# Kernel optimization log

Hardware: AMD Instinct MI355X
Metric: run time of the kernel (lower is better)

## Reference

```python
import jax, jax.numpy as jnp
import numpy as np

B, T, C, H = 2, 2048, 1024, 16
D = C // H  # head dim = 64


def setup_inputs() -> dict:
    key = jax.random.key(0)
    ks = jax.random.split(key, 9)
    s = 1.0 / np.sqrt(C)
    x = jax.random.normal(ks[0], (B, T, C), dtype=jnp.float32)
    # causal lower-triangular mask, broadcast over heads: [B, 1, T, T]
    attn_mask = jnp.broadcast_to(jnp.tril(jnp.ones((T, T), dtype=jnp.int32)), (B, 1, T, T))
    Wq = jax.random.normal(ks[1], (C, C), dtype=jnp.float32) * s
    Wk = jax.random.normal(ks[2], (C, C), dtype=jnp.float32) * s
    Wv = jax.random.normal(ks[3], (C, C), dtype=jnp.float32) * s
    Wo = jax.random.normal(ks[4], (C, C), dtype=jnp.float32) * s
    bq = jax.random.normal(ks[5], (C,), dtype=jnp.float32) * s
    bk = jax.random.normal(ks[6], (C,), dtype=jnp.float32) * s
    bv = jax.random.normal(ks[7], (C,), dtype=jnp.float32) * s
    bo = jax.random.normal(ks[8], (C,), dtype=jnp.float32) * s
    return {"x": x, "attn_mask": attn_mask, "Wq": Wq, "bq": bq, "Wk": Wk, "bk": bk,
            "Wv": Wv, "bv": bv, "Wo": Wo, "bo": bo}


def reference(x, attn_mask, Wq, bq, Wk, bk, Wv, bv, Wo, bo):
    # Q/K/V projections: nn.Linear applies x @ W^T + b
    def split_heads(t):  # [B,T,C] -> [B,H,T,D]
        return t.reshape(B, T, H, D).transpose(0, 2, 1, 3)

    q = split_heads(x @ Wq.T + bq)
    k = split_heads(x @ Wk.T + bk)
    v = split_heads(x @ Wv.T + bv)

    scale = 1.0 / np.sqrt(D)
    att = jnp.einsum('bhqd,bhkd->bhqk', q, k) * scale  # [B,H,T,T]
    att = jnp.where(attn_mask[:, :, :T, :T] == 0, -jnp.inf, att)
    att = jax.nn.softmax(att, axis=-1)
    # dropout p=0.0 -> identity
    y = jnp.einsum('bhqk,bhkd->bhqd', att, v)  # [B,H,T,D]
    y = y.transpose(0, 2, 1, 3).reshape(B, T, C)
    return y @ Wo.T + bo
```

## Files before the change

kernel.cpp:

```cpp
#include <hip/hip_runtime.h>
#include <hip/hip_bf16.h>

#define B_ 2
#define T_ 2048
#define C_ 1024
#define H_ 16
#define D_ 64
#define BT_ (B_ * T_)
#define S3_ 3072

typedef __bf16 bf16x8 __attribute__((ext_vector_type(8)));
typedef short short8v __attribute__((ext_vector_type(8)));
typedef short s16x4 __attribute__((ext_vector_type(4)));
typedef float f32x4 __attribute__((ext_vector_type(4)));

__device__ inline bf16x8 ld_frag_bf(const short* p) {
    short8v s = *(const short8v*)p;
    return __builtin_bit_cast(bf16x8, s);
}
__device__ inline short f2bf(float f) {
    union { float f; unsigned u; } x;
    x.f = f;
    unsigned r = x.u + 0x7fff + ((x.u >> 16) & 1);
    return (short)(r >> 16);
}
__device__ inline void st_out(short* p, float v) { *p = f2bf(v); }
__device__ inline void st_out(float* p, float v) { *p = v; }

__device__ inline void async16(const void* g, void* l) {
    __builtin_amdgcn_global_load_lds(
        (const __attribute__((address_space(1))) unsigned*)g,
        (__attribute__((address_space(3))) unsigned*)l, 16, 0, 0);
}

__global__ __launch_bounds__(256) void conv_inputs(
    const float* __restrict__ x,
    const float* __restrict__ Wq, const float* __restrict__ Wk,
    const float* __restrict__ Wv, const float* __restrict__ Wo,
    short* __restrict__ xb, short* __restrict__ Wqkvb, short* __restrict__ Wob)
{
    size_t e = ((size_t)blockIdx.x * 256 + threadIdx.x) * 8;
    int r = (int)(e >> 20);
    size_t off = e & ((1u << 20) - 1);
    const float* src; short* dst;
    if (r < 4)      { src = x + e;  dst = xb + e; }
    else if (r < 7) { src = (r == 4 ? Wq : r == 5 ? Wk : Wv) + off;
                      dst = Wqkvb + ((size_t)(r - 4) << 20) + off; }
    else            { src = Wo + off; dst = Wob + off; }
    f32x4 a = *(const f32x4*)src;
    f32x4 b = *(const f32x4*)(src + 4);
    short8v s;
#pragma unroll
    for (int i = 0; i < 4; ++i) { s[i] = f2bf(a[i]); s[i + 4] = f2bf(b[i]); }
    *(short8v*)dst = s;
}

__global__ __launch_bounds__(256) void gemm_qkv(
    const short* __restrict__ A,
    const short* __restrict__ Wb,
    const float* __restrict__ b0, const float* __restrict__ b1,
    const float* __restrict__ b2,
    short* __restrict__ Out, short* __restrict__ VQ)
{
    constexpr int K = 1024;
    __shared__ __align__(16) short Bs[128 * 64];
    __shared__ __align__(16) short As[128 * 64];

    const int tid = threadIdx.x;
    const int w = tid >> 6, l = tid & 63;
    const int c = l & 15, qd = l >> 4;
    const int m0 = blockIdx.y * 128, n0 = blockIdx.x * 128;
    const int wm = w >> 1, wn = w & 1;
    const int srcC = (l & 7) ^ (l >> 3);

    f32x4 acc[4][4] = {};

    for (int k0 = 0; k0 < K; k0 += 64) {
#pragma unroll
        for (int p = 0; p < 4; ++p) {
            int row = (w * 4 + p) * 8 + (l >> 3);
            async16(Wb + (size_t)(n0 + row) * K + k0 + srcC * 8,
                    Bs + (w * 4 + p) * 512 + l * 8);
            async16(A + (size_t)(m0 + row) * K + k0 + srcC * 8,
                    As + (w * 4 + p) * 512 + l * 8);
        }
        __syncthreads();

#pragma unroll
        for (int h = 0; h < 2; ++h) {
            const int slot = ((h * 4 + qd) ^ (c & 7)) * 8;
            bf16x8 af[4], bfr[4];
#pragma unroll
            for (int i = 0; i < 4; ++i) {
                af[i]  = ld_frag_bf(As + (wm * 64 + i * 16 + c) * 64 + slot);
                bfr[i] = ld_frag_bf(Bs + (wn * 64 + i * 16 + c) * 64 + slot);
            }
#pragma unroll
            for (int i = 0; i < 4; ++i)
#pragma unroll
                for (int j = 0; j < 4; ++j)
                    acc[i][j] = __builtin_amdgcn_mfma_f32_16x16x32_bf16(af[i], bfr[j], acc[i][j], 0, 0, 0);
        }
        __syncthreads();
    }

    if (n0 >= 2048) {
        const int h  = (n0 - 2048 + wn * 64) >> 6;
        const int b  = m0 >> 11;
        const int kt = ((m0 & 2047) + wm * 64) >> 6;
        short* vt = VQ + (((size_t)(b * 16 + h) * 32 + kt) * 4096);
#pragma unroll
        for (int i = 0; i < 4; ++i)
#pragma unroll
            for (int j = 0; j < 4; ++j) {
                float bv = b2[n0 - 2048 + wn * 64 + j * 16 + c];
                s16x4 st;
#pragma unroll
                for (int r = 0; r < 4; ++r) st[r] = f2bf(acc[i][j][r] + bv);
                *(s16x4*)&vt[((i * 4 + j) * 64 + qd * 16 + c) * 4] = st;
            }
    } else {
        const float* bias = (n0 < 1024) ? b0 : b1;
#pragma unroll
        for (int i = 0; i < 4; ++i)
#pragma unroll
            for (int j = 0; j < 4; ++j) {
                int n = n0 + wn * 64 + j * 16 + c;
                float bv = bias[n & 1023];
#pragma unroll
                for (int r = 0; r < 4; ++r) {
                    int m = m0 + wm * 64 + i * 16 + qd * 4 + r;
                    Out[(size_t)m * S3_ + n] = f2bf(acc[i][j][r] + bv);
                }
            }
    }
}

template <typename OT>
__global__ __launch_bounds__(256) void gemm_n64(
    const short* __restrict__ A, int lda,
    const short* __restrict__ Wb, const float* __restrict__ bias,
    OT* __restrict__ Out, int ldo)
{
    constexpr int K = 1024;
    __shared__ __align__(16) short Bs[64 * 64];
    __shared__ __align__(16) short As[128 * 64];

    const int tid = threadIdx.x;
    const int w = tid >> 6, l = tid & 63;
    const int c = l & 15, qd = l >> 4;
    const int m0 = blockIdx.y * 128, n0 = blockIdx.x * 64;
    const int wm = w >> 1, wn = w & 1;
    const int srcC = (l & 7) ^ (l >> 3);

    f32x4 acc[4][2] = {};

    for (int k0 = 0; k0 < K; k0 += 64) {
#pragma unroll
        for (int p = 0; p < 2; ++p) {
            int row = (w * 2 + p) * 8 + (l >> 3);
            async16(Wb + (size_t)(n0 + row) * K + k0 + srcC * 8,
                    Bs + (w * 2 + p) * 512 + l * 8);
        }
#pragma unroll
        for (int p = 0; p < 4; ++p) {
            int row = (w * 4 + p) * 8 + (l >> 3);
            async16(A + (size_t)(m0 + row) * lda + k0 + srcC * 8,
                    As + (w * 4 + p) * 512 + l * 8);
        }
        __syncthreads();

#pragma unroll
        for (int h = 0; h < 2; ++h) {
            const int slot = ((h * 4 + qd) ^ (c & 7)) * 8;
            bf16x8 af[4], bfr[2];
#pragma unroll
            for (int i = 0; i < 4; ++i)
                af[i] = ld_frag_bf(As + (wm * 64 + i * 16 + c) * 64 + slot);
#pragma unroll
            for (int j = 0; j < 2; ++j)
                bfr[j] = ld_frag_bf(Bs + (wn * 32 + j * 16 + c) * 64 + slot);
#pragma unroll
            for (int i = 0; i < 4; ++i)
#pragma unroll
                for (int j = 0; j < 2; ++j)
                    acc[i][j] = __builtin_amdgcn_mfma_f32_16x16x32_bf16(af[i], bfr[j], acc[i][j], 0, 0, 0);
        }
        __syncthreads();
    }

#pragma unroll
    for (int i = 0; i < 4; ++i)
#pragma unroll
        for (int j = 0; j < 2; ++j) {
            int n = n0 + wn * 32 + j * 16 + c;
            float bv = bias[n];
#pragma unroll
            for (int r = 0; r < 4; ++r) {
                int m = m0 + wm * 64 + i * 16 + qd * 4 + r;
                st_out(Out + (size_t)m * ldo + n, acc[i][j][r] + bv);
            }
        }
}

__global__ __launch_bounds__(256) void attn_flash7(
    short* __restrict__ QKV, const short* __restrict__ VQ)
{
    __shared__ __align__(16) short Ksm[2][4096];
    __shared__ __align__(16) short Vsm[2][4096];

    const int tid = threadIdx.x;
    const int w = tid >> 6, l = tid & 63;
    const int c = l & 15, qd = l >> 4;
    const int id = blockIdx.x;
    const int bh = (id & 7) * 4 + ((id >> 3) & 3);
    const int qt = 31 - (id >> 5);
    const int b = bh >> 4, h = bh & 15;
    const int sw = c & 7;

    short* Qbase = QKV + (size_t)b * T_ * S3_ + h * 64;
    const short* Kbase = Qbase + 1024;
    const short* VTb = VQ + (size_t)bh * 32 * 4096;

    const int wq0 = qt * 64 + w * 16;

    bf16x8 aq0 = ld_frag_bf(Qbase + (size_t)(wq0 + c) * S3_ + qd * 8);
    bf16x8 aq1 = ld_frag_bf(Qbase + (size_t)(wq0 + c) * S3_ + 32 + qd * 8);

    f32x4 o[4] = {};
    float lsum = 0.f;

#pragma unroll
    for (int p = 0; p < 2; ++p) {
        int row = p * 32 + w * 8 + (l >> 3);
        int srcC = (l & 7) ^ (row & 7);
        async16(Kbase + (size_t)row * S3_ + srcC * 8,
                &Ksm[0][row * 64 + (l & 7) * 8]);
        async16(VTb + p * 2048 + w * 512 + l * 8,
                &Vsm[0][p * 2048 + w * 512 + l * 8]);
    }
    __syncthreads();

#pragma unroll 1
    for (int kt = 0; kt <= qt; ++kt) {
        const int cur = kt & 1;
        const int k0 = kt * 64;

        if (kt < qt) {
            const short* vtile = VTb + (size_t)(kt + 1) * 4096;
#pragma unroll
            for (int p = 0; p < 2; ++p) {
                int row = p * 32 + w * 8 + (l >> 3);
                int srcC = (l & 7) ^ (row & 7);
                async16(Kbase + (size_t)(k0 + 64 + row) * S3_ + srcC * 8,
                        &Ksm[1 - cur][row * 64 + (l & 7) * 8]);
                async16(vtile + p * 2048 + w * 512 + l * 8,
                        &Vsm[1 - cur][p * 2048 + w * 512 + l * 8]);
            }
        }

        f32x4 st[4];
#pragma unroll
        for (int j = 0; j < 4; ++j) {
            st[j] = (f32x4){0.f, 0.f, 0.f, 0.f};
            const short* kr = &Ksm[cur][(j * 16 + c) * 64];
            bf16x8 kb0 = ld_frag_bf(kr + (qd ^ sw) * 8);
            bf16x8 kb1 = ld_frag_bf(kr + ((qd ^ 4) ^ sw) * 8);
            st[j] = __builtin_amdgcn_mfma_f32_16x16x32_bf16(kb0, aq0, st[j], 0, 0, 0);
            st[j] = __builtin_amdgcn_mfma_f32_16x16x32_bf16(kb1, aq1, st[j], 0, 0, 0);
        }

        s16x4 pb[4];
        if (kt < qt) {
#pragma unroll
            for (int j = 0; j < 4; ++j)
#pragma unroll
                for (int r = 0; r < 4; ++r) {
                    float p = __expf(fmaf(st[j][r], 0.125f, -8.0f));
                    lsum += p;
                    pb[j][r] = f2bf(p);
                }
        } else {
            const int qloc = w * 16 + c;
#pragma unroll
            for (int j = 0; j < 4; ++j)
#pragma unroll
                for (int r = 0; r < 4; ++r) {
                    float p = __expf(fmaf(st[j][r], 0.125f, -8.0f));
                    if (j * 16 + qd * 4 + r > qloc) p = 0.f;
                    lsum += p;
                    pb[j][r] = f2bf(p);
                }
        }

#pragma unroll
        for (int j = 0; j < 4; ++j)
#pragma unroll
            for (int i = 0; i < 4; ++i) {
                s16x4 vf = *(const s16x4*)&Vsm[cur][((j * 4 + i) * 64 + qd * 16 + c) * 4];
                o[i] = __builtin_amdgcn_mfma_f32_16x16x16bf16_1k(vf, pb[j], o[i], 0, 0, 0);
            }
        __syncthreads();
    }

    float lt = lsum;
    lt += __shfl_xor(lt, 16);
    lt += __shfl_xor(lt, 32);
    float inv = 1.0f / lt;

#pragma unroll
    for (int i = 0; i < 4; ++i) {
        s16x4 yb;
#pragma unroll
        for (int r = 0; r < 4; ++r) yb[r] = f2bf(o[i][r] * inv);
        *(s16x4*)&Qbase[(size_t)(wq0 + c) * S3_ + i * 16 + qd * 4] = yb;
    }
}

extern "C" void kernel_launch(void* const* d_in, const int* in_sizes, int n_in,
                              void* d_out, int out_size, void* d_ws, size_t ws_size,
                              hipStream_t stream)
{
    const float* x  = (const float*)d_in[0];
    const float* Wq = (const float*)d_in[2];
    const float* bq = (const float*)d_in[3];
    const float* Wk = (const float*)d_in[4];
    const float* bk = (const float*)d_in[5];
    const float* Wv = (const float*)d_in[6];
    const float* bv = (const float*)d_in[7];
    const float* Wo = (const float*)d_in[8];
    const float* bo = (const float*)d_in[9];
    float* out = (float*)d_out;

    short* QKVs  = (short*)d_ws;
    short* Wqkvb = QKVs + (size_t)BT_ * S3_;
    short* Wob   = Wqkvb + (size_t)S3_ * C_;
    short* xb    = (short*)d_out;
    short* VQ    = (short*)d_out + (size_t)4 * 1024 * 1024;

    conv_inputs<<<4096, 256, 0, stream>>>(x, Wq, Wk, Wv, Wo, xb, Wqkvb, Wob);
    gemm_qkv<<<dim3(S3_ / 128, BT_ / 128), 256, 0, stream>>>(
        xb, Wqkvb, bq, bk, bv, QKVs, VQ);
    attn_flash7<<<1024, 256, 0, stream>>>(QKVs, VQ);
    gemm_n64<float><<<dim3(C_ / 64, BT_ / 128), 256, 0, stream>>>(
        QKVs, S3_, Wob, bo, out, C_);
}
```

Measured before the change: 205.4 us.

## Double-buffer weight tiles in LDS and load A fragments directly from global

Both GEMM kernels now keep the weight (B) tile in a double-buffered LDS array, prefetching the next K-slice while the current one is computed, with one barrier per iteration. The A operand is no longer staged through LDS; each wave reads its MFMA fragments straight from global memory. The float-to-bf16 conversion also switches to the compiler's native cast. The aim is to overlap weight loads with MFMA work and cut LDS traffic. The cost is redundant global reads of A across the two column waves, possibly exposed global latency, and the native cast may round differently.

```diff
diff --git a/kernel.cpp b/kernel.cpp
--- a/kernel.cpp
+++ b/kernel.cpp
@@ -19,10 +19,7 @@
     return __builtin_bit_cast(bf16x8, s);
 }
 __device__ inline short f2bf(float f) {
-    union { float f; unsigned u; } x;
-    x.f = f;
-    unsigned r = x.u + 0x7fff + ((x.u >> 16) & 1);
-    return (short)(r >> 16);
+    return __builtin_bit_cast(short, (__bf16)f);
 }
 __device__ inline void st_out(short* p, float v) { *p = f2bf(v); }
 __device__ inline void st_out(float* p, float v) { *p = v; }
@@ -63,8 +60,7 @@
     short* __restrict__ Out, short* __restrict__ VQ)
 {
     constexpr int K = 1024;
-    __shared__ __align__(16) short Bs[128 * 64];
-    __shared__ __align__(16) short As[128 * 64];
+    __shared__ __align__(16) short Bs[2][128 * 64];
 
     const int tid = threadIdx.x;
     const int w = tid >> 6, l = tid & 63;
@@ -75,31 +71,48 @@
 
     f32x4 acc[4][4] = {};
 
-    for (int k0 = 0; k0 < K; k0 += 64) {
-#pragma unroll
-        for (int p = 0; p < 4; ++p) {
-            int row = (w * 4 + p) * 8 + (l >> 3);
-            async16(Wb + (size_t)(n0 + row) * K + k0 + srcC * 8,
-                    Bs + (w * 4 + p) * 512 + l * 8);
-            async16(A + (size_t)(m0 + row) * K + k0 + srcC * 8,
-                    As + (w * 4 + p) * 512 + l * 8);
-        }
-        __syncthreads();
+#pragma unroll
+    for (int p = 0; p < 4; ++p) {
+        int row = (w * 4 + p) * 8 + (l >> 3);
+        async16(Wb + (size_t)(n0 + row) * K + srcC * 8,
+                Bs[0] + (w * 4 + p) * 512 + l * 8);
+    }
+    __syncthreads();
+
+#pragma unroll 1
+    for (int it = 0; it < 16; ++it) {
+        const int k0 = it * 64;
+        const int cur = it & 1;
+
+        if (it < 15) {
+#pragma unroll
+            for (int p = 0; p < 4; ++p) {
+                int row = (w * 4 + p) * 8 + (l >> 3);
+                async16(Wb + (size_t)(n0 + row) * K + k0 + 64 + srcC * 8,
+                        Bs[1 - cur] + (w * 4 + p) * 512 + l * 8);
+            }
+        }
+
+        bf16x8 af[2][4];
+#pragma unroll
+        for (int h = 0; h < 2; ++h)
+#pragma unroll
+            for (int i = 0; i < 4; ++i)
+                af[h][i] = ld_frag_bf(A + (size_t)(m0 + wm * 64 + i * 16 + c) * K
+                                        + k0 + h * 32 + qd * 8);
 
 #pragma unroll
         for (int h = 0; h < 2; ++h) {
             const int slot = ((h * 4 + qd) ^ (c & 7)) * 8;
-            bf16x8 af[4], bfr[4];
-#pragma unroll
-            for (int i = 0; i < 4; ++i) {
-                af[i]  = ld_frag_bf(As + (wm * 64 + i * 16 + c) * 64 + slot);
-                bfr[i] = ld_frag_bf(Bs + (wn * 64 + i * 16 + c) * 64 + slot);
-            }
+            bf16x8 bfr[4];
+#pragma unroll
+            for (int j = 0; j < 4; ++j)
+                bfr[j] = ld_frag_bf(Bs[cur] + (wn * 64 + j * 16 + c) * 64 + slot);
 #pragma unroll
             for (int i = 0; i < 4; ++i)
 #pragma unroll
                 for (int j = 0; j < 4; ++j)
-                    acc[i][j] = __builtin_amdgcn_mfma_f32_16x16x32_bf16(af[i], bfr[j], acc[i][j], 0, 0, 0);
+                    acc[i][j] = __builtin_amdgcn_mfma_f32_16x16x32_bf16(af[h][i], bfr[j], acc[i][j], 0, 0, 0);
         }
         __syncthreads();
     }
@@ -143,8 +156,7 @@
     OT* __restrict__ Out, int ldo)
 {
     constexpr int K = 1024;
-    __shared__ __align__(16) short Bs[64 * 64];
-    __shared__ __align__(16) short As[128 * 64];
+    __shared__ __align__(16) short Bs[2][64 * 64];
 
     const int tid = threadIdx.x;
     const int w = tid >> 6, l = tid & 63;
@@ -155,36 +167,48 @@
 
     f32x4 acc[4][2] = {};
 
-    for (int k0 = 0; k0 < K; k0 += 64) {
-#pragma unroll
-        for (int p = 0; p < 2; ++p) {
-            int row = (w * 2 + p) * 8 + (l >> 3);
-            async16(Wb + (size_t)(n0 + row) * K + k0 + srcC * 8,
-                    Bs + (w * 2 + p) * 512 + l * 8);
-        }
-#pragma unroll
-        for (int p = 0; p < 4; ++p) {
-            int row = (w * 4 + p) * 8 + (l >> 3);
-            async16(A + (size_t)(m0 + row) * lda + k0 + srcC * 8,
-                    As + (w * 4 + p) * 512 + l * 8);
-        }
-        __syncthreads();
+#pragma unroll
+    for (int p = 0; p < 2; ++p) {
+        int row = (w * 2 + p) * 8 + (l >> 3);
+        async16(Wb + (size_t)(n0 + row) * K + srcC * 8,
+                Bs[0] + (w * 2 + p) * 512 + l * 8);
+    }
+    __syncthreads();
+
+#pragma unroll 1
+    for (int it = 0; it < 16; ++it) {
+        const int k0 = it * 64;
+        const int cur = it & 1;
+
+        if (it < 15) {
+#pragma unroll
+            for (int p = 0; p < 2; ++p) {
+                int row = (w * 2 + p) * 8 + (l >> 3);
+                async16(Wb + (size_t)(n0 + row) * K + k0 + 64 + srcC * 8,
+                        Bs[1 - cur] + (w * 2 + p) * 512 + l * 8);
+            }
+        }
+
+        bf16x8 af[2][4];
+#pragma unroll
+        for (int h = 0; h < 2; ++h)
+#pragma unroll
+            for (int i = 0; i < 4; ++i)
+                af[h][i] = ld_frag_bf(A + (size_t)(m0 + wm * 64 + i * 16 + c) * lda
+                                        + k0 + h * 32 + qd * 8);
 
 #pragma unroll
         for (int h = 0; h < 2; ++h) {
             const int slot = ((h * 4 + qd) ^ (c & 7)) * 8;
-            bf16x8 af[4], bfr[2];
+            bf16x8 bfr[2];
+#pragma unroll
+            for (int j = 0; j < 2; ++j)
+                bfr[j] = ld_frag_bf(Bs[cur] + (wn * 32 + j * 16 + c) * 64 + slot);
 #pragma unroll
             for (int i = 0; i < 4; ++i)
-                af[i] = ld_frag_bf(As + (wm * 64 + i * 16 + c) * 64 + slot);
-#pragma unroll
-            for (int j = 0; j < 2; ++j)
-                bfr[j] = ld_frag_bf(Bs + (wn * 32 + j * 16 + c) * 64 + slot);
-#pragma unroll
-            for (int i = 0; i < 4; ++i)
 #pragma unroll
                 for (int j = 0; j < 2; ++j)
-                    acc[i][j] = __builtin_amdgcn_mfma_f32_16x16x32_bf16(af[i], bfr[j], acc[i][j], 0, 0, 0);
+                    acc[i][j] = __builtin_amdgcn_mfma_f32_16x16x32_bf16(af[h][i], bfr[j], acc[i][j], 0, 0, 0);
         }
         __syncthreads();
     }
```

New measurement: 260.1 us. 1.27x slower.
